# Performance work log

Hardware: AMD Instinct MI355X
Metric: run time of the kernel (lower is better)

## Reference

```python
import jax, jax.numpy as jnp
import numpy as np

NEG_BIG = -10000.0  # matches torch.full((S,S), -10000.0) causal mask

def setup_inputs() -> dict:
    key = jax.random.key(0)
    kq, kk, kv = jax.random.split(key, 3)
    B, S, H, D = 2, 2048, 16, 64
    q = jax.random.normal(kq, (B, S, H, D), dtype=jnp.float32)
    k = jax.random.normal(kk, (B, S, H, D), dtype=jnp.float32)
    v = jax.random.normal(kv, (B, S, H, D), dtype=jnp.float32)
    return {"q": q, "k": k, "v": v}

def reference(q, k, v):
    # q,k,v: [B, S, H, D]
    S = q.shape[1]
    scale = 1.0 / jnp.sqrt(jnp.asarray(q.shape[-1], q.dtype))
    scores = jnp.einsum('bthd,bshd->bhts', q, k * scale)  # [B,H,S,S]
    causal_mask = jnp.triu(jnp.full((S, S), NEG_BIG, dtype=scores.dtype), 1)
    scores = scores + causal_mask  # broadcast over B,H
    attn = jax.nn.softmax(scores, axis=-1).astype(v.dtype)
    # dropout_p = 0.0, so dropout is identity
    out = jnp.einsum('bhts,bshd->bthd', attn, v)  # [B,S,H,D]
    return out
```

## Files before the change

### kernel.cpp

```cpp
#include <hip/hip_runtime.h>

#define LOG2E 1.4426950408889634f
#define EXP2(x) __builtin_amdgcn_exp2f(x)
#define MFMA32(a, b, c) __builtin_amdgcn_mfma_f32_32x32x16_bf16(a, b, c, 0, 0, 0)

typedef __attribute__((ext_vector_type(4)))  float f32x4;
typedef __attribute__((ext_vector_type(16))) float f32x16;
typedef __attribute__((ext_vector_type(8)))  short s16x8;
typedef __attribute__((ext_vector_type(4)))  short s16x4;
typedef __attribute__((ext_vector_type(4)))  __bf16 bf16x4;
typedef __attribute__((ext_vector_type(8)))  __bf16 bf16x8;

#define SS 2048
#define HH 16
#define DD 64
#define HSZ (HH * DD)
#define BHSZ (SS * DD)

__global__ __launch_bounds__(256) void prep_kv16(const float* __restrict__ Kg,
                                                 const float* __restrict__ Vg,
                                                 short* __restrict__ Kf,
                                                 short* __restrict__ Vf) {
  __shared__ float tile[128][65];
  const int tid = threadIdx.x;
  const int blk = blockIdx.x;
  const int isV = blk >> 9;
  const int local = blk & 511;
  const int bh  = local >> 4;
  const int grp = local & 15;
  const int b = bh >> 4, h = bh & 15;
  const float* __restrict__ src = isV ? Vg : Kg;

#pragma unroll
  for (int p = 0; p < 8; ++p) {
    const int row = p * 16 + (tid >> 4);
    const int d4  = (tid & 15) << 2;
    const int key = (grp << 7) + row;
    f32x4 v = *(const f32x4*)(src + (((size_t)b * SS + key) * HH + h) * DD + d4);
    tile[row][d4] = v[0];
    tile[row][d4 + 1] = v[1];
    tile[row][d4 + 2] = v[2];
    tile[row][d4 + 3] = v[3];
  }
  __syncthreads();

  if (!isV) {
#pragma unroll
    for (int it = 0; it < 4; ++it) {
      const int id = it * 256 + tid;
      const int l  = id & 63;
      const int c2 = (id >> 6) & 3;
      const int sl = (id >> 8) & 3;
      const int keyl = (sl << 5) + (l & 31);
      const int d0   = (c2 << 4) + ((l >> 5) << 3);
      bf16x8 o;
#pragma unroll
      for (int j = 0; j < 8; ++j) o[j] = (__bf16)tile[keyl][d0 + j];
      const size_t chunk = (((size_t)bh * 64 + ((grp << 2) + sl)) * 4 + c2) * 64 + l;
      *(s16x8*)(Kf + chunk * 8) = __builtin_bit_cast(s16x8, o);
    }
  } else {
#pragma unroll
    for (int it = 0; it < 4; ++it) {
      const int id = it * 256 + tid;
      const int l  = id & 63;
      const int kh = (id >> 6) & 1;
      const int db = (id >> 7) & 1;
      const int sl = (id >> 8) & 3;
      const int d   = (db << 5) + (l & 31);
      const int hi4 = (l >> 5) << 2;
      bf16x8 o;
#pragma unroll
      for (int j = 0; j < 8; ++j) {
        const int keyl = (sl << 5) + (kh << 4) + ((j & 3) + ((j >> 2) << 3) + hi4);
        o[j] = (__bf16)tile[keyl][d];
      }
      const size_t chunk =
          ((((size_t)bh * 64 + ((grp << 2) + sl)) * 2 + db) * 2 + kh) * 64 + l;
      *(s16x8*)(Vf + chunk * 8) = __builtin_bit_cast(s16x8, o);
    }
  }
}


__global__ __launch_bounds__(256, 4) void attn_fwd17(
    const float* __restrict__ Qg, const short* __restrict__ Kf,
    const short* __restrict__ Vf, float* __restrict__ Og)
{
  __shared__ float lo[2][33][64];

  const int tid  = threadIdx.x;
  const int lane = tid & 63;
  const int w    = tid >> 6;
  const int lm31 = lane & 31;
  const int hi   = lane >> 5;

  const int id   = blockIdx.x;
  const int xcd  = id & 7;
  const int r8   = id >> 3;
  const int bh   = (xcd << 2) | (r8 & 3);
  const int t    = 63 - (r8 >> 2);
  const int n    = t + 1;

  const size_t qbase = (size_t)(bh >> 4) * SS * HSZ + (size_t)(bh & 15) * DD;
  const short* kb2 = Kf + (size_t)bh * BHSZ + lane * 8;
  const short* vb2 = Vf + (size_t)bh * BHSZ + lane * 8;

  s16x8 qf[4];
  {
    const float qs = 0.125f * LOG2E;
    const float* qp = Qg + qbase + (size_t)((t << 5) + lm31) * HSZ + (hi << 3);
#pragma unroll
    for (int c2 = 0; c2 < 4; ++c2) {
      f32x4 a = *(const f32x4*)(qp + c2 * 16);
      f32x4 b2 = *(const f32x4*)(qp + c2 * 16 + 4);
      bf16x8 bv;
#pragma unroll
      for (int j = 0; j < 4; ++j) {
        bv[j] = (__bf16)(a[j] * qs);
        bv[4 + j] = (__bf16)(b2[j] * qs);
      }
      qf[c2] = __builtin_bit_cast(s16x8, bv);
    }
  }

  f32x16 oacc0 = {0,0,0,0,0,0,0,0,0,0,0,0,0,0,0,0};
  f32x16 oacc1 = {0,0,0,0,0,0,0,0,0,0,0,0,0,0,0,0};
  float lsum = 0.0f;

  const int n4 = n >> 2, rem = n & 3;
  int s = w * n4 + (w < rem ? w : rem);
  const int e = s + n4 + (w < rem ? 1 : 0);

  for (; s < e; ++s) {
    const short* ka = kb2 + ((size_t)s << 11);
    s16x8 k0 = *(const s16x8*)(ka);
    s16x8 k1 = *(const s16x8*)(ka + 512);
    f32x16 st = {0,0,0,0,0,0,0,0,0,0,0,0,0,0,0,0};
    st = MFMA32(k0, qf[0], st);
    st = MFMA32(k1, qf[1], st);
    s16x8 k2 = *(const s16x8*)(ka + 1024);
    s16x8 k3 = *(const s16x8*)(ka + 1536);
    st = MFMA32(k2, qf[2], st);
    st = MFMA32(k3, qf[3], st);
    if (s == t) {
#pragma unroll
      for (int r = 0; r < 16; ++r)
        if (((r & 3) + ((r >> 2) << 3) + (hi << 2)) > lm31) st[r] = -1e30f;
    }
    float p[16];
#pragma unroll
    for (int r = 0; r < 16; ++r) p[r] = EXP2(st[r]);
    {
      const float s0 = (p[0] + p[1]) + (p[2] + p[3]);
      const float s1 = (p[4] + p[5]) + (p[6] + p[7]);
      const float s2 = (p[8] + p[9]) + (p[10] + p[11]);
      const float s3 = (p[12] + p[13]) + (p[14] + p[15]);
      lsum += (s0 + s1) + (s2 + s3);
    }
    bf16x8 pb0, pb1;
#pragma unroll
    for (int r = 0; r < 8; ++r) {
      pb0[r] = (__bf16)p[r];
      pb1[r] = (__bf16)p[8 + r];
    }
    const s16x8 pf0 = __builtin_bit_cast(s16x8, pb0);
    const s16x8 pf1 = __builtin_bit_cast(s16x8, pb1);
    const short* vpp = vb2 + ((size_t)s << 11);
    s16x8 va00 = *(const s16x8*)(vpp);
    s16x8 va01 = *(const s16x8*)(vpp + 512);
    s16x8 va10 = *(const s16x8*)(vpp + 1024);
    s16x8 va11 = *(const s16x8*)(vpp + 1536);
    oacc0 = MFMA32(va00, pf0, oacc0);
    oacc0 = MFMA32(va01, pf1, oacc0);
    oacc1 = MFMA32(va10, pf0, oacc1);
    oacc1 = MFMA32(va11, pf1, oacc1);
  }

  if (w == 1 || w == 3) {
    const int slot = w >> 1;
#pragma unroll
    for (int r = 0; r < 16; ++r) {
      lo[slot][r][lane] = oacc0[r];
      lo[slot][16 + r][lane] = oacc1[r];
    }
    lo[slot][32][lane] = lsum;
  }
  __syncthreads();
  if (w == 0) {
#pragma unroll
    for (int r = 0; r < 16; ++r) {
      oacc0[r] += lo[0][r][lane];
      oacc1[r] += lo[0][16 + r][lane];
    }
    lsum += lo[0][32][lane];
  }
  if (w == 2) {
#pragma unroll
    for (int r = 0; r < 16; ++r) {
      oacc0[r] += lo[1][r][lane];
      oacc1[r] += lo[1][16 + r][lane];
    }
    lsum += lo[1][32][lane];
#pragma unroll
    for (int r = 0; r < 16; ++r) {
      lo[1][r][lane] = oacc0[r];
      lo[1][16 + r][lane] = oacc1[r];
    }
    lo[1][32][lane] = lsum;
  }
  __syncthreads();
  if (w == 0) {
#pragma unroll
    for (int r = 0; r < 16; ++r) {
      oacc0[r] += lo[1][r][lane];
      oacc1[r] += lo[1][16 + r][lane];
    }
    lsum += lo[1][32][lane];
    float l = lsum + __shfl_xor(lsum, 32);
    const float inv = 1.0f / l;
    float* op = Og + qbase + (size_t)((t << 5) + lm31) * HSZ + (hi << 2);
#pragma unroll
    for (int db = 0; db < 2; ++db)
#pragma unroll
      for (int q4 = 0; q4 < 4; ++q4) {
        f32x4 o;
#pragma unroll
        for (int j = 0; j < 4; ++j)
          o[j] = (db ? oacc1[q4 * 4 + j] : oacc0[q4 * 4 + j]) * inv;
        *(f32x4*)(op + db * 32 + q4 * 8) = o;
      }
  }
}

__global__ __launch_bounds__(256) void attn_fwd(
    const float* __restrict__ Qg, const float* __restrict__ Kg,
    const float* __restrict__ Vg, float* __restrict__ Og)
{
  typedef __attribute__((ext_vector_type(4))) short s16x4v;
  const int tid  = threadIdx.x;
  const int lane = tid & 63;
  const int lm   = lane & 15;
  const int g    = lane >> 4;
  const int w    = tid >> 6;
  const int bh = blockIdx.x;
  const int b  = bh >> 4;
  const int h  = bh & 15;
  const int t  = ((gridDim.y - 1 - blockIdx.y) << 2) | w;
  const int qb = t << 4;
  const size_t base = (size_t)b * SS * HSZ + (size_t)h * DD;
  s16x4v qf[4];
  {
    const float* qp = Qg + base + (size_t)(qb + lm) * HSZ + g * 4;
    const float qs = 0.125f * LOG2E;
#pragma unroll
    for (int c = 0; c < 4; ++c) {
      f32x4 qv = *(const f32x4*)(qp + c * 16);
      bf16x4 bv;
#pragma unroll
      for (int j = 0; j < 4; ++j) bv[j] = (__bf16)(qv[j] * qs);
      qf[c] = __builtin_bit_cast(s16x4v, bv);
    }
  }
  f32x4 oacc[4] = {{0,0,0,0},{0,0,0,0},{0,0,0,0},{0,0,0,0}};
  float m = -1e30f, lsum = 0.0f;
  const float* kp = Kg + base + (size_t)lm * HSZ + g * 4;
  const float* vp = Vg + base + (size_t)(g * 4) * HSZ + lm;
  for (int kt = 0; kt <= t; ++kt) {
    const float* kpp = kp + (size_t)(kt << 4) * HSZ;
    f32x4 st = {0, 0, 0, 0};
#pragma unroll
    for (int c = 0; c < 4; ++c) {
      f32x4 kv = *(const f32x4*)(kpp + c * 16);
      bf16x4 bv;
#pragma unroll
      for (int j = 0; j < 4; ++j) bv[j] = (__bf16)kv[j];
      st = __builtin_amdgcn_mfma_f32_16x16x16bf16_1k(
               __builtin_bit_cast(s16x4v, bv), qf[c], st, 0, 0, 0);
    }
    if (kt == t) {
#pragma unroll
      for (int r = 0; r < 4; ++r)
        if (g * 4 + r > lm) st[r] = -1e30f;
    }
    float tmax = fmaxf(fmaxf(st[0], st[1]), fmaxf(st[2], st[3]));
    tmax = fmaxf(tmax, __shfl_xor(tmax, 16));
    tmax = fmaxf(tmax, __shfl_xor(tmax, 32));
    const float mnew = fmaxf(m, tmax);
    const float fsc  = exp2f(m - mnew);
    f32x4 p;
#pragma unroll
    for (int r = 0; r < 4; ++r) p[r] = exp2f(st[r] - mnew);
    float tsum = (p[0] + p[1]) + (p[2] + p[3]);
    tsum += __shfl_xor(tsum, 16);
    tsum += __shfl_xor(tsum, 32);
    lsum = lsum * fsc + tsum;
    m = mnew;
#pragma unroll
    for (int nb = 0; nb < 4; ++nb)
#pragma unroll
      for (int r = 0; r < 4; ++r) oacc[nb][r] *= fsc;
    bf16x4 pb;
#pragma unroll
    for (int r = 0; r < 4; ++r) pb[r] = (__bf16)p[r];
    const s16x4v pf = __builtin_bit_cast(s16x4v, pb);
    const float* vpp = vp + (size_t)(kt << 4) * HSZ;
#pragma unroll
    for (int nb = 0; nb < 4; ++nb) {
      bf16x4 vv;
#pragma unroll
      for (int j = 0; j < 4; ++j)
        vv[j] = (__bf16)vpp[(size_t)j * HSZ + nb * 16];
      oacc[nb] = __builtin_amdgcn_mfma_f32_16x16x16bf16_1k(
                     __builtin_bit_cast(s16x4v, vv), pf, oacc[nb], 0, 0, 0);
    }
  }
  const float inv = 1.0f / lsum;
  float* op = Og + base + (size_t)(qb + lm) * HSZ + g * 4;
#pragma unroll
  for (int nb = 0; nb < 4; ++nb) {
    f32x4 o = oacc[nb];
#pragma unroll
    for (int r = 0; r < 4; ++r) o[r] *= inv;
    *(f32x4*)(op + nb * 16) = o;
  }
}

extern "C" void kernel_launch(void* const* d_in, const int* in_sizes, int n_in,
                              void* d_out, int out_size, void* d_ws, size_t ws_size,
                              hipStream_t stream) {
  const float* q = (const float*)d_in[0];
  const float* k = (const float*)d_in[1];
  const float* v = (const float*)d_in[2];
  float* o = (float*)d_out;
  const size_t elems = (size_t)2 * HH * SS * DD;
  const size_t need  = 2 * elems * sizeof(short);
  if (ws_size >= need) {
    short* Kf = (short*)d_ws;
    short* Vf = Kf + elems;
    prep_kv16<<<1024, 256, 0, stream>>>(k, v, Kf, Vf);
    attn_fwd17<<<2048, 256, 0, stream>>>(q, Kf, Vf, o);
  } else {
    attn_fwd<<<dim3(32, 32), 256, 0, stream>>>(q, k, v, o);
  }
}
```

Before: 44.85 us.

## Split long causal query tiles across two blocks with a separate merge kernel

```diff
diff --git a/kernel.cpp b/kernel.cpp
--- a/kernel.cpp
+++ b/kernel.cpp
@@ -83,24 +83,42 @@
 }
 
 
-__global__ __launch_bounds__(256, 4) void attn_fwd17(
+__global__ __launch_bounds__(256, 4) void attn_fwd18(
     const float* __restrict__ Qg, const short* __restrict__ Kf,
-    const short* __restrict__ Vf, float* __restrict__ Og)
+    const short* __restrict__ Vf, float* __restrict__ Pbuf,
+    float* __restrict__ Og)
 {
-  __shared__ float lo[2][33][64];
+  __shared__ float lsm[2][33][64];
 
   const int tid  = threadIdx.x;
   const int lane = tid & 63;
   const int w    = tid >> 6;
   const int lm31 = lane & 31;
-  const int hi   = lane >> 5;
+  const int hb   = lane >> 5;
 
   const int id   = blockIdx.x;
   const int xcd  = id & 7;
-  const int r8   = id >> 3;
-  const int bh   = (xcd << 2) | (r8 & 3);
-  const int t    = 63 - (r8 >> 2);
-  const int n    = t + 1;
+  const int rest = id >> 3;
+  const int bh   = (xcd << 2) | (rest & 3);
+  const int tau  = rest >> 2;
+  const int gidx = tau / 3;
+  const int r3   = tau - gidx * 3;
+  int t, klo, khi, pidx;
+  bool part;
+  if (r3 < 2) {
+    t = 63 - gidx;
+    const int h = (t + 1) >> 1;
+    part = true;
+    klo = r3 ? h : 0;
+    khi = r3 ? (t + 1) : h;
+    pidx = bh * 64 + (t - 32) * 2 + r3;
+  } else {
+    t = 31 - gidx;
+    part = false;
+    klo = 0;
+    khi = t + 1;
+    pidx = 0;
+  }
 
   const size_t qbase = (size_t)(bh >> 4) * SS * HSZ + (size_t)(bh & 15) * DD;
   const short* kb2 = Kf + (size_t)bh * BHSZ + lane * 8;
@@ -109,7 +127,7 @@
   s16x8 qf[4];
   {
     const float qs = 0.125f * LOG2E;
-    const float* qp = Qg + qbase + (size_t)((t << 5) + lm31) * HSZ + (hi << 3);
+    const float* qp = Qg + qbase + (size_t)((t << 5) + lm31) * HSZ + (hb << 3);
 #pragma unroll
     for (int c2 = 0; c2 < 4; ++c2) {
       f32x4 a = *(const f32x4*)(qp + c2 * 16);
@@ -128,8 +146,9 @@
   f32x16 oacc1 = {0,0,0,0,0,0,0,0,0,0,0,0,0,0,0,0};
   float lsum = 0.0f;
 
-  const int n4 = n >> 2, rem = n & 3;
-  int s = w * n4 + (w < rem ? w : rem);
+  const int len = khi - klo;
+  const int n4 = len >> 2, rem = len & 3;
+  int s = klo + w * n4 + (w < rem ? w : rem);
   const int e = s + n4 + (w < rem ? 1 : 0);
 
   for (; s < e; ++s) {
@@ -146,7 +165,7 @@
     if (s == t) {
 #pragma unroll
       for (int r = 0; r < 16; ++r)
-        if (((r & 3) + ((r >> 2) << 3) + (hi << 2)) > lm31) st[r] = -1e30f;
+        if (((r & 3) + ((r >> 2) << 3) + (hb << 2)) > lm31) st[r] = -1e30f;
     }
     float p[16];
 #pragma unroll
@@ -177,6 +196,195 @@
     oacc1 = MFMA32(va11, pf1, oacc1);
   }
 
+  if (w == 1 || w == 3) {
+    const int slot = w >> 1;
+#pragma unroll
+    for (int r = 0; r < 16; ++r) {
+      lsm[slot][r][lane] = oacc0[r];
+      lsm[slot][16 + r][lane] = oacc1[r];
+    }
+    lsm[slot][32][lane] = lsum;
+  }
+  __syncthreads();
+  if (w == 0) {
+#pragma unroll
+    for (int r = 0; r < 16; ++r) {
+      oacc0[r] += lsm[0][r][lane];
+      oacc1[r] += lsm[0][16 + r][lane];
+    }
+    lsum += lsm[0][32][lane];
+  }
+  if (w == 2) {
+#pragma unroll
+    for (int r = 0; r < 16; ++r) {
+      oacc0[r] += lsm[1][r][lane];
+      oacc1[r] += lsm[1][16 + r][lane];
+    }
+    lsum += lsm[1][32][lane];
+#pragma unroll
+    for (int r = 0; r < 16; ++r) {
+      lsm[1][r][lane] = oacc0[r];
+      lsm[1][16 + r][lane] = oacc1[r];
+    }
+    lsm[1][32][lane] = lsum;
+  }
+  __syncthreads();
+  if (w == 0) {
+#pragma unroll
+    for (int r = 0; r < 16; ++r) {
+      oacc0[r] += lsm[1][r][lane];
+      oacc1[r] += lsm[1][16 + r][lane];
+    }
+    lsum += lsm[1][32][lane];
+    if (part) {
+      float* pp = Pbuf + (size_t)pidx * (33 * 64);
+#pragma unroll
+      for (int r = 0; r < 16; ++r) {
+        pp[r * 64 + lane] = oacc0[r];
+        pp[(16 + r) * 64 + lane] = oacc1[r];
+      }
+      pp[32 * 64 + lane] = lsum;
+    } else {
+      float l = lsum + __shfl_xor(lsum, 32);
+      const float inv = 1.0f / l;
+      float* op = Og + qbase + (size_t)((t << 5) + lm31) * HSZ + (hb << 2);
+#pragma unroll
+      for (int db = 0; db < 2; ++db)
+#pragma unroll
+        for (int q4 = 0; q4 < 4; ++q4) {
+          f32x4 o;
+#pragma unroll
+          for (int j = 0; j < 4; ++j)
+            o[j] = (db ? oacc1[q4 * 4 + j] : oacc0[q4 * 4 + j]) * inv;
+          *(f32x4*)(op + db * 32 + q4 * 8) = o;
+        }
+    }
+  }
+}
+
+__global__ __launch_bounds__(64) void merge18(const float* __restrict__ Pbuf,
+                                              float* __restrict__ Og) {
+  const int id   = blockIdx.x;
+  const int lane = threadIdx.x;
+  const int bh = id >> 5;
+  const int ht = id & 31;
+  const int t  = ht + 32;
+  const int lm31 = lane & 31;
+  const int hb   = lane >> 5;
+
+  const float* p0 = Pbuf + (size_t)(bh * 64 + ht * 2) * (33 * 64);
+  const float* p1 = p0 + 33 * 64;
+
+  float o0[16], o1[16];
+#pragma unroll
+  for (int r = 0; r < 16; ++r) {
+    o0[r] = p0[r * 64 + lane] + p1[r * 64 + lane];
+    o1[r] = p0[(16 + r) * 64 + lane] + p1[(16 + r) * 64 + lane];
+  }
+  float ls = p0[32 * 64 + lane] + p1[32 * 64 + lane];
+  ls += __shfl_xor(ls, 32);
+  const float inv = 1.0f / ls;
+
+  const size_t qbase = (size_t)(bh >> 4) * SS * HSZ + (size_t)(bh & 15) * DD;
+  float* op = Og + qbase + (size_t)((t << 5) + lm31) * HSZ + (hb << 2);
+#pragma unroll
+  for (int db = 0; db < 2; ++db)
+#pragma unroll
+    for (int q4 = 0; q4 < 4; ++q4) {
+      f32x4 o;
+#pragma unroll
+      for (int j = 0; j < 4; ++j)
+        o[j] = (db ? o1[q4 * 4 + j] : o0[q4 * 4 + j]) * inv;
+      *(f32x4*)(op + db * 32 + q4 * 8) = o;
+    }
+}
+
+__global__ __launch_bounds__(256, 4) void attn_fwd17(
+    const float* __restrict__ Qg, const short* __restrict__ Kf,
+    const short* __restrict__ Vf, float* __restrict__ Og)
+{
+  __shared__ float lo[2][33][64];
+  const int tid  = threadIdx.x;
+  const int lane = tid & 63;
+  const int w    = tid >> 6;
+  const int lm31 = lane & 31;
+  const int hi   = lane >> 5;
+  const int id   = blockIdx.x;
+  const int xcd  = id & 7;
+  const int r8   = id >> 3;
+  const int bh   = (xcd << 2) | (r8 & 3);
+  const int t    = 63 - (r8 >> 2);
+  const int n    = t + 1;
+  const size_t qbase = (size_t)(bh >> 4) * SS * HSZ + (size_t)(bh & 15) * DD;
+  const short* kb2 = Kf + (size_t)bh * BHSZ + lane * 8;
+  const short* vb2 = Vf + (size_t)bh * BHSZ + lane * 8;
+  s16x8 qf[4];
+  {
+    const float qs = 0.125f * LOG2E;
+    const float* qp = Qg + qbase + (size_t)((t << 5) + lm31) * HSZ + (hi << 3);
+#pragma unroll
+    for (int c2 = 0; c2 < 4; ++c2) {
+      f32x4 a = *(const f32x4*)(qp + c2 * 16);
+      f32x4 b2 = *(const f32x4*)(qp + c2 * 16 + 4);
+      bf16x8 bv;
+#pragma unroll
+      for (int j = 0; j < 4; ++j) {
+        bv[j] = (__bf16)(a[j] * qs);
+        bv[4 + j] = (__bf16)(b2[j] * qs);
+      }
+      qf[c2] = __builtin_bit_cast(s16x8, bv);
+    }
+  }
+  f32x16 oacc0 = {0,0,0,0,0,0,0,0,0,0,0,0,0,0,0,0};
+  f32x16 oacc1 = {0,0,0,0,0,0,0,0,0,0,0,0,0,0,0,0};
+  float lsum = 0.0f;
+  const int n4 = n >> 2, rem = n & 3;
+  int s = w * n4 + (w < rem ? w : rem);
+  const int e = s + n4 + (w < rem ? 1 : 0);
+  for (; s < e; ++s) {
+    const short* ka = kb2 + ((size_t)s << 11);
+    s16x8 k0 = *(const s16x8*)(ka);
+    s16x8 k1 = *(const s16x8*)(ka + 512);
+    f32x16 st = {0,0,0,0,0,0,0,0,0,0,0,0,0,0,0,0};
+    st = MFMA32(k0, qf[0], st);
+    st = MFMA32(k1, qf[1], st);
+    s16x8 k2 = *(const s16x8*)(ka + 1024);
+    s16x8 k3 = *(const s16x8*)(ka + 1536);
+    st = MFMA32(k2, qf[2], st);
+    st = MFMA32(k3, qf[3], st);
+    if (s == t) {
+#pragma unroll
+      for (int r = 0; r < 16; ++r)
+        if (((r & 3) + ((r >> 2) << 3) + (hi << 2)) > lm31) st[r] = -1e30f;
+    }
+    float p[16];
+#pragma unroll
+    for (int r = 0; r < 16; ++r) p[r] = EXP2(st[r]);
+    {
+      const float s0 = (p[0] + p[1]) + (p[2] + p[3]);
+      const float s1 = (p[4] + p[5]) + (p[6] + p[7]);
+      const float s2 = (p[8] + p[9]) + (p[10] + p[11]);
+      const float s3 = (p[12] + p[13]) + (p[14] + p[15]);
+      lsum += (s0 + s1) + (s2 + s3);
+    }
+    bf16x8 pb0, pb1;
+#pragma unroll
+    for (int r = 0; r < 8; ++r) {
+      pb0[r] = (__bf16)p[r];
+      pb1[r] = (__bf16)p[8 + r];
+    }
+    const s16x8 pf0 = __builtin_bit_cast(s16x8, pb0);
+    const s16x8 pf1 = __builtin_bit_cast(s16x8, pb1);
+    const short* vpp = vb2 + ((size_t)s << 11);
+    s16x8 va00 = *(const s16x8*)(vpp);
+    s16x8 va01 = *(const s16x8*)(vpp + 512);
+    s16x8 va10 = *(const s16x8*)(vpp + 1024);
+    s16x8 va11 = *(const s16x8*)(vpp + 1536);
+    oacc0 = MFMA32(va00, pf0, oacc0);
+    oacc0 = MFMA32(va01, pf1, oacc0);
+    oacc1 = MFMA32(va10, pf0, oacc1);
+    oacc1 = MFMA32(va11, pf1, oacc1);
+  }
   if (w == 1 || w == 3) {
     const int slot = w >> 1;
 #pragma unroll
@@ -333,9 +541,17 @@
   const float* k = (const float*)d_in[1];
   const float* v = (const float*)d_in[2];
   float* o = (float*)d_out;
-  const size_t elems = (size_t)2 * HH * SS * DD;
-  const size_t need  = 2 * elems * sizeof(short);
-  if (ws_size >= need) {
+  const size_t elems  = (size_t)2 * HH * SS * DD;
+  const size_t kvneed = 2 * elems * sizeof(short);
+  const size_t pneed  = (size_t)2048 * 33 * 64 * 4;
+  if (ws_size >= kvneed + pneed) {
+    short* Kf = (short*)d_ws;
+    short* Vf = Kf + elems;
+    float* Pbuf = (float*)((char*)d_ws + kvneed);
+    prep_kv16<<<1024, 256, 0, stream>>>(k, v, Kf, Vf);
+    attn_fwd18<<<3072, 256, 0, stream>>>(q, Kf, Vf, Pbuf, o);
+    merge18<<<1024, 64, 0, stream>>>(Pbuf, o);
+  } else if (ws_size >= kvneed) {
     short* Kf = (short*)d_ws;
     short* Vf = Kf + elems;
     prep_kv16<<<1024, 256, 0, stream>>>(k, v, Kf, Vf);
```

Result: slower. 55.60 us (+24.0%).
